# Optimization experiments

Measured on AMD Instinct MI355X. Metric: run time of the kernel, lower is better.

Reference implementation:

```python
import jax, jax.numpy as jnp
import numpy as np
from jax import lax

EPOCHS, P, IN_SIZE, OUT_SIZE = 3, 8, 32, 16
BS, C_EEG, T = 256, 22, 1000
DN = ('NCHW', 'OIHW', 'NCHW')


def _bn(h, g, b):
    # BatchNorm2d in training mode: biased batch stats over (N, H, W)
    mu = h.mean(axis=(0, 2, 3), keepdims=True)
    var = ((h - mu) ** 2).mean(axis=(0, 2, 3), keepdims=True)
    return (h - mu) * lax.rsqrt(var + 1e-5) * g.reshape(1, -1, 1, 1) + b.reshape(1, -1, 1, 1)


def _forward(x, conv1_w, conv1_b, bn1_g, bn1_b, conv2_w, conv2_b, bn2_g, bn2_b,
             wq, wk, wv, lin_w, lin_b):
    h = lax.conv_general_dilated(x, conv1_w, (1, 1), 'VALID', dimension_numbers=DN)
    h = jax.nn.elu(_bn(h + conv1_b.reshape(1, -1, 1, 1), bn1_g, bn1_b))          # (B,22,1,T)
    h = lax.conv_general_dilated(h, conv2_w, (1, 1), 'VALID', dimension_numbers=DN)
    h = jax.nn.elu(_bn(h + conv2_b.reshape(1, -1, 1, 1), bn2_g, bn2_b))          # (B,96,1,T-11)
    h = h[:, :, 0, :]                                                            # squeeze -> (B,96,T2)
    bs = h.shape[0]
    # E2R: split channel axis into EPOCHS equal patches, Projmap = X X^T
    X = h.reshape(bs, EPOCHS, IN_SIZE, -1)                                       # (B,m,32,T2)
    S = jnp.einsum('bmct,bmdt->bmcd', X, X)                                      # (B,m,32,32) SPD
    # Orthmap(p): top-p eigenvectors of S
    _, U = jnp.linalg.eigh(S)
    Up = U[..., ::-1][..., :P]                                                   # (B,m,32,8)
    # AttentionManifold: FRMap (W @ X) then QR composition -> orthonormal frames
    Q = jnp.linalg.qr(jnp.einsum('oi,bmip->bmop', wq, Up))[0]                    # (B,m,16,8)
    K = jnp.linalg.qr(jnp.einsum('oi,bmip->bmop', wk, Up))[0]
    V = jnp.linalg.qr(jnp.einsum('oi,bmip->bmop', wv, Up))[0]
    # projection-metric energy: E[b,i,j] = ||D D^T||_F with D = Q_j Q_j^T - K_i K_i^T
    QQt = jnp.einsum('bjdp,bjep->bjde', Q, Q)                                    # (B,m,16,16)
    KKt = jnp.einsum('bidp,biep->bide', K, K)
    D = QQt[:, None] - KKt[:, :, None]                                           # (B,i,j,16,16)
    E = jnp.sqrt(jnp.sum(jnp.matmul(D, jnp.swapaxes(D, -1, -2)) ** 2, axis=(-2, -1)))
    B = jax.nn.softmax(1.0 / (1.0 + jnp.log1p(E)), axis=1).transpose(0, 2, 1)    # (B,m,m)
    Vp = jnp.einsum('bmdp,bmep->bmde', V, V)                                     # Projmap(V)
    # faithful to the source triple loop: last j overwrites -> out[b,i] = B[b,i,-1] * Vp[b,-1]
    out = B[:, :, -1][:, :, None, None] * Vp[:, -1][:, None]                     # (B,m,16,16)
    return out.reshape(bs, -1) @ lin_w.T + lin_b                                 # (B,4)


def setup_inputs() -> dict:
    key = jax.random.key(0)
    ks = jax.random.split(key, 8)
    d2 = EPOCHS * IN_SIZE
    return {
        'x': jax.random.normal(ks[0], (BS, 1, C_EEG, T), jnp.float32),
        'conv1_w': jax.random.normal(ks[1], (C_EEG, 1, C_EEG, 1), jnp.float32) * 0.1,
        'conv1_b': jnp.zeros((C_EEG,), jnp.float32),
        'bn1_g': jnp.ones((C_EEG,), jnp.float32),
        'bn1_b': jnp.zeros((C_EEG,), jnp.float32),
        'conv2_w': jax.random.normal(ks[2], (d2, C_EEG, 1, 12), jnp.float32) * 0.05,
        'conv2_b': jnp.zeros((d2,), jnp.float32),
        'bn2_g': jnp.ones((d2,), jnp.float32),
        'bn2_b': jnp.zeros((d2,), jnp.float32),
        'wq': jax.random.normal(ks[3], (OUT_SIZE, IN_SIZE), jnp.float32) * 0.2,
        'wk': jax.random.normal(ks[4], (OUT_SIZE, IN_SIZE), jnp.float32) * 0.2,
        'wv': jax.random.normal(ks[5], (OUT_SIZE, IN_SIZE), jnp.float32) * 0.2,
        'lin_w': jax.random.normal(ks[6], (4, EPOCHS * OUT_SIZE * OUT_SIZE), jnp.float32) * 0.05,
        'lin_b': jnp.zeros((4,), jnp.float32),
    }


def reference(x, conv1_w, conv1_b, bn1_g, bn1_b, conv2_w, conv2_b, bn2_g, bn2_b,
              wq, wk, wv, lin_w, lin_b):
    return _forward(x, conv1_w, conv1_b, bn1_g, bn1_b, conv2_w, conv2_b, bn2_g, bn2_b,
                    wq, wk, wv, lin_w, lin_b)
```

## Files before the change

kernel.cpp:

```cpp
#include <hip/hip_runtime.h>
#include <math.h>

#define PDIM 8
#define BSZ 256
#define CEEG 22
#define TLEN 1000
#define KW 12
#define C2 96
#define TOUT 989
#define TSTR 992
#define NSWEEP 5
#define NT8 8
#define NPART (BSZ*NT8*2)

typedef __attribute__((ext_vector_type(8))) short short8;
typedef __attribute__((ext_vector_type(4))) float floatx4;

#define OFF_H1   ((size_t)0)
#define SZ_H1    ((size_t)BSZ*CEEG*TLEN)
#define OFF_H2   (OFF_H1 + SZ_H1)
#define SZ_H2    ((size_t)BSZ*C2*TSTR)
#define OFF_S    (OFF_H2 + SZ_H2)
#define SZ_S     ((size_t)BSZ*3*1024)
#define OFF_WH   (OFF_S)
#define OFF_WL   (OFF_S + (size_t)13824)
#define OFF_QQT  (OFF_S + SZ_S)
#define SZ_QQT   ((size_t)BSZ*3*256)
#define OFF_KKT  (OFF_QQT + SZ_QQT)
#define OFF_VP   (OFF_KKT + SZ_QQT)
#define SZ_VP    ((size_t)BSZ*256)
#define OFF_P1   (OFF_VP + SZ_VP)
#define SZ_P1    ((size_t)BSZ*44)
#define OFF_P2   (OFF_P1 + SZ_P1)
#define SZ_P2    ((size_t)NPART*192)
#define OFF_BN1  (OFF_P2 + SZ_P2)
#define OFF_BN2  (OFF_BN1 + (size_t)64)

__device__ __forceinline__ float elu_f(float z) { return z > 0.f ? z : expm1f(z); }

__device__ __forceinline__ unsigned short f2bf(float x) {
    unsigned u = __float_as_uint(x);
    u += 0x7fffu + ((u >> 16) & 1u);
    return (unsigned short)(u >> 16);
}
__device__ __forceinline__ float bf2f(unsigned short h) {
    return __uint_as_float(((unsigned)h) << 16);
}

__global__ __launch_bounds__(256) void k0_wsplit(const float* __restrict__ w2,
        unsigned short* __restrict__ Whi, unsigned short* __restrict__ Wlo) {
    int i = blockIdx.x*256 + threadIdx.x;
    if (i >= 96*288) return;
    int o = i / 288, kap = i - o*288;
    float v = (kap < 264) ? w2[o*264 + kap] : 0.f;
    unsigned short h = f2bf(v);
    float lo = v - bf2f(h);
    Whi[i] = h;
    Wlo[i] = f2bf(lo);
}

__global__ __launch_bounds__(256) void k1_conv1(const float* __restrict__ x,
        const float* __restrict__ w1, float* __restrict__ h1,
        float* __restrict__ part1) {
    __shared__ float sw[CEEG*CEEG];
    __shared__ float red[4][44];
    int b = blockIdx.x;
    int tid = threadIdx.x;
    for (int i = tid; i < CEEG*CEEG; i += 256) sw[i] = w1[i];
    __syncthreads();
    float sum[CEEG], sumsq[CEEG];
    #pragma unroll
    for (int o = 0; o < CEEG; ++o) { sum[o] = 0.f; sumsq[o] = 0.f; }
    const float* xb = x + (size_t)b*CEEG*TLEN;
    float* hb = h1 + (size_t)b*CEEG*TLEN;
    for (int it = 0; it < 4; ++it) {
        int t = it*256 + tid;
        if (t < TLEN) {
            float acc[CEEG];
            #pragma unroll
            for (int o = 0; o < CEEG; ++o) acc[o] = 0.f;
            #pragma unroll 2
            for (int c = 0; c < CEEG; ++c) {
                float xv = xb[c*TLEN + t];
                #pragma unroll
                for (int o = 0; o < CEEG; ++o) acc[o] = fmaf(xv, sw[o*CEEG + c], acc[o]);
            }
            #pragma unroll
            for (int o = 0; o < CEEG; ++o) {
                hb[o*TLEN + t] = acc[o];
                sum[o]  += acc[o];
                sumsq[o] += acc[o]*acc[o];
            }
        }
    }
    int lane = tid & 63, wv = tid >> 6;
    #pragma unroll
    for (int o = 0; o < CEEG; ++o) {
        float s = sum[o], s2 = sumsq[o];
        for (int off = 32; off > 0; off >>= 1) {
            s  += __shfl_down(s,  off, 64);
            s2 += __shfl_down(s2, off, 64);
        }
        if (lane == 0) { red[wv][o] = s; red[wv][CEEG + o] = s2; }
    }
    __syncthreads();
    if (tid < 44) {
        part1[(size_t)b*44 + tid] = red[0][tid] + red[1][tid] + red[2][tid] + red[3][tid];
    }
}

__global__ __launch_bounds__(64) void k2_bn1(const float* __restrict__ part1,
        const float* __restrict__ g, const float* __restrict__ bta, float* __restrict__ p1) {
    int c = blockIdx.x, t = threadIdx.x;
    float s = 0.f, s2 = 0.f;
    for (int blk = t; blk < BSZ; blk += 64) {
        s  += part1[(size_t)blk*44 + c];
        s2 += part1[(size_t)blk*44 + CEEG + c];
    }
    for (int off = 32; off > 0; off >>= 1) {
        s  += __shfl_down(s,  off, 64);
        s2 += __shfl_down(s2, off, 64);
    }
    if (t == 0) {
        double N = (double)BSZ * (double)TLEN;
        double mu = (double)s / N, var = (double)s2 / N - mu*mu;
        double scale = (double)g[c] / sqrt(var + 1e-5);
        p1[c] = (float)scale;
        p1[CEEG + c] = (float)((double)bta[c] - mu*scale);
    }
}

__global__ __launch_bounds__(256) void k3_conv2(const float* __restrict__ h1,
        const unsigned short* __restrict__ WhiG, const unsigned short* __restrict__ WloG,
        const float* __restrict__ p1, float* __restrict__ h2, float* __restrict__ part2) {
    __shared__ unsigned Epack[22*152];
    __shared__ unsigned short ctab[288];
    __shared__ short XhiL[128*40];
    __shared__ short XloL[128*40];
    int b = blockIdx.x;
    int tile = blockIdx.y;
    int t0 = tile * 128;
    int tid = threadIdx.x;
    int lane = tid & 63, w = tid >> 6;
    int r16 = lane & 15, q = lane >> 4;
    int mg = w & 1, ng = w >> 1;
    const float* hb = h1 + (size_t)b*CEEG*TLEN;

    for (int i = tid; i < 22*139; i += 256) {
        int c = i / 139, tt = i - c*139;
        int t = t0 + tt;
        unsigned pk = 0u;
        if (t < TLEN) {
            float v = elu_f(fmaf(hb[c*TLEN + t], p1[c], p1[CEEG + c]));
            unsigned uv = __float_as_uint(v);
            unsigned hi = uv & 0xFFFF0000u;
            float lo = v - __uint_as_float(hi);
            pk = hi | (__float_as_uint(lo) >> 16);
        }
        Epack[c*152 + tt] = pk;
    }
    for (int i = tid; i < 288; i += 256) {
        int c = i / 12, k = i - c*12;
        ctab[i] = (i < 264) ? (unsigned short)(c*152 + k) : (unsigned short)0xFFFF;
    }

    const unsigned short* ahP[3];
    const unsigned short* alP[3];
    #pragma unroll
    for (int m = 0; m < 3; ++m) {
        int row = mg*48 + m*16 + r16;
        ahP[m] = WhiG + row*288 + q*8;
        alP[m] = WloG + row*288 + q*8;
    }
    short8 ahC[3], alC[3];
    #pragma unroll
    for (int m = 0; m < 3; ++m) {
        ahC[m] = *(const short8*)&ahP[m][0];
        alC[m] = *(const short8*)&alP[m][0];
    }

    floatx4 acc[3][4];
    #pragma unroll
    for (int m = 0; m < 3; ++m)
        #pragma unroll
        for (int nf = 0; nf < 4; ++nf) acc[m][nf] = (floatx4){0.f, 0.f, 0.f, 0.f};

    __syncthreads();

    #pragma unroll
    for (int s = 0; s < 2; ++s) {
        int u = tid + s*256;
        int t = u >> 2, c4 = u & 3;
        const unsigned short* ct = &ctab[c4*8];
        unsigned dh[4], dl[4];
        #pragma unroll
        for (int jp = 0; jp < 4; ++jp) {
            unsigned short o0 = ct[2*jp], o1 = ct[2*jp+1];
            unsigned p0 = (o0 != 0xFFFFu) ? Epack[o0 + t] : 0u;
            unsigned p1v = (o1 != 0xFFFFu) ? Epack[o1 + t] : 0u;
            dh[jp] = (p0 >> 16) | (p1v & 0xFFFF0000u);
            dl[jp] = (p0 << 16 >> 16) | (p1v << 16);
        }
        *(uint4*)&XhiL[t*40 + c4*8] = make_uint4(dh[0], dh[1], dh[2], dh[3]);
        *(uint4*)&XloL[t*40 + c4*8] = make_uint4(dl[0], dl[1], dl[2], dl[3]);
    }
    __syncthreads();

    for (int kc = 0; kc < 9; ++kc) {
        short8 ahN[3], alN[3];
        if (kc + 1 < 9) {
            #pragma unroll
            for (int m = 0; m < 3; ++m) {
                ahN[m] = *(const short8*)&ahP[m][(kc+1)*32];
                alN[m] = *(const short8*)&alP[m][(kc+1)*32];
            }
        }
        #pragma unroll
        for (int nf = 0; nf < 4; ++nf) {
            int tn = (ng*4 + nf)*16 + r16;
            short8 bh = *(const short8*)&XhiL[tn*40 + q*8];
            short8 bl = *(const short8*)&XloL[tn*40 + q*8];
            #pragma unroll
            for (int m = 0; m < 3; ++m) {
                acc[m][nf] = __builtin_amdgcn_mfma_f32_16x16x32_bf16(ahC[m], bh, acc[m][nf], 0, 0, 0);
                acc[m][nf] = __builtin_amdgcn_mfma_f32_16x16x32_bf16(ahC[m], bl, acc[m][nf], 0, 0, 0);
                acc[m][nf] = __builtin_amdgcn_mfma_f32_16x16x32_bf16(alC[m], bh, acc[m][nf], 0, 0, 0);
            }
        }
        if (kc + 1 < 9) {
            __syncthreads();
            #pragma unroll
            for (int s = 0; s < 2; ++s) {
                int u = tid + s*256;
                int t = u >> 2, c4 = u & 3;
                const unsigned short* ct = &ctab[(kc+1)*32 + c4*8];
                unsigned dh[4], dl[4];
                #pragma unroll
                for (int jp = 0; jp < 4; ++jp) {
                    unsigned short o0 = ct[2*jp], o1 = ct[2*jp+1];
                    unsigned p0 = (o0 != 0xFFFFu) ? Epack[o0 + t] : 0u;
                    unsigned p1v = (o1 != 0xFFFFu) ? Epack[o1 + t] : 0u;
                    dh[jp] = (p0 >> 16) | (p1v & 0xFFFF0000u);
                    dl[jp] = (p0 << 16 >> 16) | (p1v << 16);
                }
                *(uint4*)&XhiL[t*40 + c4*8] = make_uint4(dh[0], dh[1], dh[2], dh[3]);
                *(uint4*)&XloL[t*40 + c4*8] = make_uint4(dl[0], dl[1], dl[2], dl[3]);
            }
            __syncthreads();
            #pragma unroll
            for (int m = 0; m < 3; ++m) { ahC[m] = ahN[m]; alC[m] = alN[m]; }
        }
    }

    float* h2b = h2 + (size_t)b*C2*TSTR;
    float* pb = part2 + (((size_t)b*NT8 + tile)*2 + ng)*192;
    #pragma unroll
    for (int m = 0; m < 3; ++m) {
        float s[4] = {0.f, 0.f, 0.f, 0.f}, s2[4] = {0.f, 0.f, 0.f, 0.f};
        #pragma unroll
        for (int nf = 0; nf < 4; ++nf) {
            int t = t0 + (ng*4 + nf)*16 + r16;
            bool ok = t < TOUT;
            #pragma unroll
            for (int reg = 0; reg < 4; ++reg) {
                float v = acc[m][nf][reg];
                if (ok) {
                    int o = mg*48 + m*16 + q*4 + reg;
                    h2b[(size_t)o*TSTR + t] = v;
                    s[reg] += v; s2[reg] += v*v;
                }
            }
        }
        #pragma unroll
        for (int reg = 0; reg < 4; ++reg) {
            float a = s[reg], b2 = s2[reg];
            #pragma unroll
            for (int d = 8; d > 0; d >>= 1) {
                a  += __shfl_down(a,  d, 16);
                b2 += __shfl_down(b2, d, 16);
            }
            if (r16 == 0) {
                int o = mg*48 + m*16 + q*4 + reg;
                pb[o] = a; pb[96 + o] = b2;
            }
        }
    }
}

__global__ __launch_bounds__(256) void k4_bn2(const float* __restrict__ part2,
        const float* __restrict__ g, const float* __restrict__ bta, float* __restrict__ p2) {
    __shared__ float rs[4], rs2[4];
    int q = blockIdx.x, t = threadIdx.x;
    float s = 0.f, s2 = 0.f;
    for (int blk = t; blk < NPART; blk += 256) {
        s  += part2[(size_t)blk*192 + q];
        s2 += part2[(size_t)blk*192 + 96 + q];
    }
    for (int off = 32; off > 0; off >>= 1) {
        s  += __shfl_down(s,  off, 64);
        s2 += __shfl_down(s2, off, 64);
    }
    int lane = t & 63, wv = t >> 6;
    if (lane == 0) { rs[wv] = s; rs2[wv] = s2; }
    __syncthreads();
    if (t == 0) {
        double S  = (double)rs[0]  + rs[1]  + rs[2]  + rs[3];
        double S2 = (double)rs2[0] + rs2[1] + rs2[2] + rs2[3];
        double N = (double)BSZ * (double)TOUT;
        double mu = S / N, var = S2 / N - mu*mu;
        double scale = (double)g[q] / sqrt(var + 1e-5);
        p2[q] = (float)scale;
        p2[C2 + q] = (float)((double)bta[q] - mu*scale);
    }
}

__global__ __launch_bounds__(256) void k5_gram(const float* __restrict__ h2,
        const float* __restrict__ p2, float* __restrict__ S) {
    __shared__ float smem[4*2176];
    int bm = blockIdx.x;
    int b = bm / 3, m = bm % 3;
    int tid = threadIdx.x;
    int w = tid >> 6, lane = tid & 63;
    float* sx = smem + w*2176;
    const float* hb = h2 + ((size_t)b*C2 + m*32)*TSTR;
    int srow = lane >> 1;
    int scol = (lane & 1) * 32;
    float sc = p2[m*32 + srow], sh = p2[C2 + m*32 + srow];
    int r0 = (lane >> 3) << 2, c0 = (lane & 7) << 2;
    float acc[4][4];
    #pragma unroll
    for (int i = 0; i < 4; ++i)
        #pragma unroll
        for (int j = 0; j < 4; ++j) acc[i][j] = 0.f;

    for (int t0 = w*64; t0 < TOUT; t0 += 256) {
        const float* src = &hb[(size_t)srow*TSTR + t0 + scol];
        float* drow = &sx[srow*68 + scol];
        if (t0 + 63 < TOUT) {
            #pragma unroll
            for (int j = 0; j < 8; ++j) {
                float4 xv = *(const float4*)&src[4*j];
                float4 v;
                v.x = elu_f(fmaf(xv.x, sc, sh));
                v.y = elu_f(fmaf(xv.y, sc, sh));
                v.z = elu_f(fmaf(xv.z, sc, sh));
                v.w = elu_f(fmaf(xv.w, sc, sh));
                *(float4*)&drow[4*j] = v;
            }
        } else {
            #pragma unroll
            for (int j = 0; j < 8; ++j) {
                float4 xv = *(const float4*)&src[4*j];
                int tb = t0 + scol + 4*j;
                float4 v;
                v.x = (tb + 0 < TOUT) ? elu_f(fmaf(xv.x, sc, sh)) : 0.f;
                v.y = (tb + 1 < TOUT) ? elu_f(fmaf(xv.y, sc, sh)) : 0.f;
                v.z = (tb + 2 < TOUT) ? elu_f(fmaf(xv.z, sc, sh)) : 0.f;
                v.w = (tb + 3 < TOUT) ? elu_f(fmaf(xv.w, sc, sh)) : 0.f;
                *(float4*)&drow[4*j] = v;
            }
        }
        #pragma unroll
        for (int tc = 0; tc < 16; ++tc) {
            float4 a0 = *(const float4*)&sx[(r0+0)*68 + tc*4];
            float4 a1 = *(const float4*)&sx[(r0+1)*68 + tc*4];
            float4 a2 = *(const float4*)&sx[(r0+2)*68 + tc*4];
            float4 a3 = *(const float4*)&sx[(r0+3)*68 + tc*4];
            float4 b0 = *(const float4*)&sx[(c0+0)*68 + tc*4];
            float4 b1 = *(const float4*)&sx[(c0+1)*68 + tc*4];
            float4 b2 = *(const float4*)&sx[(c0+2)*68 + tc*4];
            float4 b3 = *(const float4*)&sx[(c0+3)*68 + tc*4];
            #pragma unroll
            for (int i = 0; i < 4; ++i) {
                float4 ai = (i == 0) ? a0 : (i == 1) ? a1 : (i == 2) ? a2 : a3;
                acc[i][0] = fmaf(ai.x, b0.x, fmaf(ai.y, b0.y, fmaf(ai.z, b0.z, fmaf(ai.w, b0.w, acc[i][0]))));
                acc[i][1] = fmaf(ai.x, b1.x, fmaf(ai.y, b1.y, fmaf(ai.z, b1.z, fmaf(ai.w, b1.w, acc[i][1]))));
                acc[i][2] = fmaf(ai.x, b2.x, fmaf(ai.y, b2.y, fmaf(ai.z, b2.z, fmaf(ai.w, b2.w, acc[i][2]))));
                acc[i][3] = fmaf(ai.x, b3.x, fmaf(ai.y, b3.y, fmaf(ai.z, b3.z, fmaf(ai.w, b3.w, acc[i][3]))));
            }
        }
    }

    float* red = smem + w*2176;
    #pragma unroll
    for (int i = 0; i < 4; ++i)
        #pragma unroll
        for (int j = 0; j < 4; ++j)
            red[lane*17 + i*4 + j] = acc[i][j];
    __syncthreads();
    int e0 = tid * 4;
    int r = e0 >> 5, c = e0 & 31;
    int tl = (r >> 2)*8 + (c >> 2);
    int sb = (r & 3)*4;
    float o0 = 0.f, o1 = 0.f, o2 = 0.f, o3 = 0.f;
    #pragma unroll
    for (int ww = 0; ww < 4; ++ww) {
        const float* rp = smem + ww*2176 + tl*17 + sb;
        o0 += rp[0]; o1 += rp[1]; o2 += rp[2]; o3 += rp[3];
    }
    float* Sb2 = S + (size_t)bm*1024;
    *(float4*)&Sb2[e0] = make_float4(o0, o1, o2, o3);
}

__device__ __forceinline__ void pair_of(int r, int k, int& p, int& q) {
    if (k == 0) { p = r; q = 31; }
    else {
        int a = (r + k) % 31;
        int b2 = (r - k + 31) % 31;
        p = min(a, b2); q = max(a, b2);
    }
}

__global__ __launch_bounds__(256) void k6_eig(const float* __restrict__ S,
        const float* __restrict__ wq, const float* __restrict__ wk, const float* __restrict__ wv,
        float* __restrict__ QQt, float* __restrict__ KKt, float* __restrict__ Vp) {
    __shared__ float A[32][35];
    __shared__ float Vt[32][34];
    __shared__ float2 cs2[16];
    __shared__ float sW[3][512];
    __shared__ unsigned int ptab[31*16];
    __shared__ float Up[32][9];
    __shared__ float Aw[16][9];
    __shared__ float G[8][9];
    __shared__ float Lm[8][9];
    __shared__ float Mm[16][9];
    __shared__ float lam[32];
    int bm = blockIdx.x, b = bm / 3, m = bm % 3;
    int tid = threadIdx.x;
    const float* Sb = S + (size_t)bm*1024;
    for (int i = tid; i < 1024; i += 256) {
        int r_ = i >> 5, c_ = i & 31;
        A[r_][c_] = Sb[i];
        Vt[r_][c_] = (r_ == c_) ? 1.f : 0.f;
    }
    for (int i = tid; i < 512; i += 256) {
        sW[0][i] = wq[i]; sW[1][i] = wk[i]; sW[2][i] = wv[i];
    }
    for (int i = tid; i < 31*16; i += 256) {
        int r_ = i >> 4, k_ = i & 15;
        int p, q; pair_of(r_, k_, p, q);
        ptab[i] = (unsigned)p | ((unsigned)q << 16);
    }
    __syncthreads();

    int kk_ = tid >> 4, ll_ = tid & 15;
    int i0 = kk_ * 2;
    for (int sweep = 0; sweep < NSWEEP; ++sweep) {
        for (int r = 0; r < 31; ++r) {
            if (tid < 16) {
                unsigned pq = ptab[(r << 4) + tid];
                int p = pq & 0xffff, q = pq >> 16;
                float app = A[p][p], aqq = A[q][q], apq = A[p][q];
                float c = 1.f, s = 0.f;
                if (apq != 0.f) {
                    float tau = (aqq - app) / (2.f * apq);
                    float tt = (tau >= 0.f ? 1.f : -1.f) / (fabsf(tau) + sqrtf(1.f + tau*tau));
                    c = 1.f / sqrtf(1.f + tt*tt);
                    s = tt * c;
                    if (!(c == c) || !(s == s)) { c = 1.f; s = 0.f; }
                }
                cs2[tid] = make_float2(c, s);
            }
            __syncthreads();
            {
                unsigned pqk = ptab[(r << 4) + kk_];
                unsigned pql = ptab[(r << 4) + ll_];
                int p = pqk & 0xffff, q = pqk >> 16;
                int rr = pql & 0xffff, ss = pql >> 16;
                float2 ck2 = cs2[kk_], cl2 = cs2[ll_];
                float ck = ck2.x, sk = ck2.y, cl = cl2.x, sl = cl2.y;
                float apr = A[p][rr], aps = A[p][ss], aqr = A[q][rr], aqs = A[q][ss];
                float tpr = ck*apr - sk*aqr;
                float tqr = sk*apr + ck*aqr;
                float tps = ck*aps - sk*aqs;
                float tqs = sk*aps + ck*aqs;
                A[p][rr] = cl*tpr - sl*tps;
                A[p][ss] = sl*tpr + cl*tps;
                A[q][rr] = cl*tqr - sl*tqs;
                A[q][ss] = sl*tqr + cl*tqs;
                float2 vr = *(const float2*)&Vt[rr][i0];
                float2 vs = *(const float2*)&Vt[ss][i0];
                float2 nvr, nvs;
                nvr.x = cl*vr.x - sl*vs.x;
                nvr.y = cl*vr.y - sl*vs.y;
                nvs.x = sl*vr.x + cl*vs.x;
                nvs.y = sl*vr.y + cl*vs.y;
                *(float2*)&Vt[rr][i0] = nvr;
                *(float2*)&Vt[ss][i0] = nvs;
            }
            __syncthreads();
        }
    }

    if (tid < 32) lam[tid] = A[tid][tid];
    __syncthreads();
    if (tid < 32) {
        float lj = lam[tid];
        int rank = 0;
        #pragma unroll
        for (int i = 0; i < 32; ++i) {
            float li = lam[i];
            rank += (li > lj) || (li == lj && i < tid);
        }
        if (rank < PDIM) {
            #pragma unroll
            for (int i = 0; i < 32; ++i) Up[i][rank] = Vt[tid][i];
        }
    }
    __syncthreads();

    for (int widx = 0; widx < 3; ++widx) {
        if (widx == 2 && m != 2) break;
        const float* W = sW[widx];
        if (tid < 128) {
            int o = tid >> 3, pp = tid & 7;
            float s = 0.f;
            #pragma unroll
            for (int i = 0; i < 32; ++i) s = fmaf(W[o*32 + i], Up[i][pp], s);
            Aw[o][pp] = s;
        }
        __syncthreads();
        if (tid < 64) {
            int xx = tid >> 3, yy = tid & 7;
            float s = 0.f;
            #pragma unroll
            for (int o = 0; o < 16; ++o) s = fmaf(Aw[o][xx], Aw[o][yy], s);
            G[xx][yy] = s;
        }
        __syncthreads();
        if (tid == 0) {
            float Lr[8][8];
            #pragma unroll
            for (int jj = 0; jj < 8; ++jj) {
                float d = G[jj][jj];
                #pragma unroll
                for (int kk = 0; kk < 8; ++kk) if (kk < jj) d -= Lr[jj][kk]*Lr[jj][kk];
                d = sqrtf(fmaxf(d, 1e-30f));
                float inv = 1.f / d;
                Lr[jj][jj] = d;
                Lm[jj][jj] = inv;
                #pragma unroll
                for (int ii = 0; ii < 8; ++ii) if (ii > jj) {
                    float v = G[ii][jj];
                    #pragma unroll
                    for (int kk = 0; kk < 8; ++kk) if (kk < jj) v -= Lr[ii][kk]*Lr[jj][kk];
                    v *= inv;
                    Lr[ii][jj] = v;
                    Lm[ii][jj] = v;
                }
            }
        }
        __syncthreads();
        if (tid < 16) {
            int o = tid;
            float a[8], mv[8];
            #pragma unroll
            for (int pp = 0; pp < 8; ++pp) a[pp] = Aw[o][pp];
            #pragma unroll
            for (int jj = 0; jj < 8; ++jj) {
                float v = a[jj];
                #pragma unroll
                for (int kk = 0; kk < 8; ++kk) if (kk < jj) v -= Lm[jj][kk]*mv[kk];
                mv[jj] = v * Lm[jj][jj];
            }
            #pragma unroll
            for (int pp = 0; pp < 8; ++pp) Mm[o][pp] = mv[pp];
        }
        __syncthreads();
        {
            int d = tid >> 4, e = tid & 15;
            float s = 0.f;
            #pragma unroll
            for (int pp = 0; pp < 8; ++pp) s = fmaf(Mm[d][pp], Mm[e][pp], s);
            float* dst = (widx == 0) ? (QQt + (size_t)bm*256)
                       : (widx == 1) ? (KKt + (size_t)bm*256)
                       : (Vp + (size_t)b*256);
            dst[d*16 + e] = s;
        }
        __syncthreads();
    }
}

__global__ __launch_bounds__(64) void k7_out(const float* __restrict__ QQt,
        const float* __restrict__ KKt, const float* __restrict__ Vp,
        const float* __restrict__ lw, const float* __restrict__ lb,
        float* __restrict__ out) {
    __shared__ float sQ[3][256], sK[3][256], sVp[256], ssc[9], wj[3];
    int b = blockIdx.x, tid = threadIdx.x;
    for (int i = tid; i < 768; i += 64) {
        sQ[i >> 8][i & 255] = QQt[(size_t)b*768 + i];
        sK[i >> 8][i & 255] = KKt[(size_t)b*768 + i];
    }
    for (int i = tid; i < 256; i += 64) sVp[i] = Vp[(size_t)b*256 + i];
    __syncthreads();
    for (int pair = 0; pair < 9; ++pair) {
        int i = pair / 3, j = pair % 3;
        const float* Qj = sQ[j];
        const float* Ki = sK[i];
        float accp = 0.f;
        #pragma unroll
        for (int it = 0; it < 4; ++it) {
            int e = tid + 64*it;
            int d = e >> 4, ee = e & 15;
            float y = 0.f;
            #pragma unroll
            for (int f = 0; f < 16; ++f) {
                float dv = Qj[d*16 + f] - Ki[d*16 + f];
                float ev = Qj[ee*16 + f] - Ki[ee*16 + f];
                y = fmaf(dv, ev, y);
            }
            accp += y*y;
        }
        for (int off = 32; off > 0; off >>= 1) accp += __shfl_down(accp, off, 64);
        if (tid == 0) {
            float E = sqrtf(accp);
            ssc[pair] = 1.f / (1.f + log1pf(E));
        }
        __syncthreads();
    }
    if (tid < 3) {
        int j = tid;
        float e0 = expf(ssc[0*3 + j]), e1 = expf(ssc[1*3 + j]), e2 = expf(ssc[2*3 + j]);
        wj[j] = e2 / (e0 + e1 + e2);
    }
    __syncthreads();
    int o = tid >> 4, g = tid & 15;
    float part = 0.f;
    #pragma unroll
    for (int t = 0; t < 16; ++t) {
        int de = g*16 + t;
        float vv = sVp[de];
        float l0 = lw[o*768 + de];
        float l1 = lw[o*768 + 256 + de];
        float l2 = lw[o*768 + 512 + de];
        part = fmaf(vv, fmaf(wj[0], l0, fmaf(wj[1], l1, wj[2]*l2)), part);
    }
    for (int off = 8; off > 0; off >>= 1) part += __shfl_down(part, off, 16);
    if (g == 0) out[b*4 + o] = part + lb[o];
}

extern "C" void kernel_launch(void* const* d_in, const int* in_sizes, int n_in,
                              void* d_out, int out_size, void* d_ws, size_t ws_size,
                              hipStream_t stream) {
    const float* x  = (const float*)d_in[0];
    const float* w1 = (const float*)d_in[1];
    const float* g1 = (const float*)d_in[3];
    const float* b1 = (const float*)d_in[4];
    const float* w2 = (const float*)d_in[5];
    const float* g2 = (const float*)d_in[7];
    const float* b2 = (const float*)d_in[8];
    const float* wq = (const float*)d_in[9];
    const float* wk = (const float*)d_in[10];
    const float* wv = (const float*)d_in[11];
    const float* lw = (const float*)d_in[12];
    const float* lb = (const float*)d_in[13];

    float* ws   = (float*)d_ws;
    float* h1   = ws + OFF_H1;
    float* h2   = ws + OFF_H2;
    float* Sm   = ws + OFF_S;
    unsigned short* WhiG = (unsigned short*)(ws + OFF_WH);
    unsigned short* WloG = (unsigned short*)(ws + OFF_WL);
    float* qqt  = ws + OFF_QQT;
    float* kkt  = ws + OFF_KKT;
    float* vpm  = ws + OFF_VP;
    float* p1a  = ws + OFF_P1;
    float* p2a  = ws + OFF_P2;
    float* bn1p = ws + OFF_BN1;
    float* bn2p = ws + OFF_BN2;

    k0_wsplit<<<(96*288 + 255)/256, 256, 0, stream>>>(w2, WhiG, WloG);
    k1_conv1<<<BSZ, 256, 0, stream>>>(x, w1, h1, p1a);
    k2_bn1<<<CEEG, 64, 0, stream>>>(p1a, g1, b1, bn1p);
    dim3 g3(BSZ, NT8);
    k3_conv2<<<g3, 256, 0, stream>>>(h1, WhiG, WloG, bn1p, h2, p2a);
    k4_bn2<<<C2, 256, 0, stream>>>(p2a, g2, b2, bn2p);
    k5_gram<<<BSZ*3, 256, 0, stream>>>(h2, bn2p, Sm);
    k6_eig<<<BSZ*3, 256, 0, stream>>>(Sm, wq, wk, wv, qqt, kkt, vpm);
    k7_out<<<BSZ, 64, 0, stream>>>(qqt, kkt, vpm, lw, lb, (float*)d_out);
}
```

Measured before the change: 386.4 us.

## Shrink Jacobi eigen kernel to a single 64-thread wavefront per matrix

Runs the per-matrix Jacobi eigensolver with 64 threads (one wavefront) instead of 256. Each thread now applies four column rotations, and the downstream FRMap, Gram and outer-product steps are remapped to fit 64 threads. The intent is to make the two block barriers per rotation round cheap, since a single-wave block needs no cross-wave synchronisation, and to fit more blocks per CU. In exchange each thread does serial work per round and there is less parallelism inside a block.

```diff
diff --git a/kernel.cpp b/kernel.cpp
--- a/kernel.cpp
+++ b/kernel.cpp
@@ -411,7 +411,7 @@
     }
 }
 
-__global__ __launch_bounds__(256) void k6_eig(const float* __restrict__ S,
+__global__ __launch_bounds__(64) void k6_eig(const float* __restrict__ S,
         const float* __restrict__ wq, const float* __restrict__ wk, const float* __restrict__ wv,
         float* __restrict__ QQt, float* __restrict__ KKt, float* __restrict__ Vp) {
     __shared__ float A[32][35];
@@ -428,29 +428,30 @@
     int bm = blockIdx.x, b = bm / 3, m = bm % 3;
     int tid = threadIdx.x;
     const float* Sb = S + (size_t)bm*1024;
-    for (int i = tid; i < 1024; i += 256) {
+    for (int i = tid; i < 1024; i += 64) {
         int r_ = i >> 5, c_ = i & 31;
         A[r_][c_] = Sb[i];
         Vt[r_][c_] = (r_ == c_) ? 1.f : 0.f;
     }
-    for (int i = tid; i < 512; i += 256) {
+    for (int i = tid; i < 512; i += 64) {
         sW[0][i] = wq[i]; sW[1][i] = wk[i]; sW[2][i] = wv[i];
     }
-    for (int i = tid; i < 31*16; i += 256) {
+    for (int i = tid; i < 31*16; i += 64) {
         int r_ = i >> 4, k_ = i & 15;
         int p, q; pair_of(r_, k_, p, q);
         ptab[i] = (unsigned)p | ((unsigned)q << 16);
     }
     __syncthreads();
 
-    int kk_ = tid >> 4, ll_ = tid & 15;
-    int i0 = kk_ * 2;
+    int kk = tid >> 2, j4 = tid & 3;
+    int i0 = kk * 2;
     for (int sweep = 0; sweep < NSWEEP; ++sweep) {
         for (int r = 0; r < 31; ++r) {
-            if (tid < 16) {
-                unsigned pq = ptab[(r << 4) + tid];
-                int p = pq & 0xffff, q = pq >> 16;
-                float app = A[p][p], aqq = A[q][q], apq = A[p][q];
+            const unsigned* pt = &ptab[r << 4];
+            {
+                unsigned pq = pt[tid & 15];
+                int p_ = pq & 0xffff, q_ = pq >> 16;
+                float app = A[p_][p_], aqq = A[q_][q_], apq = A[p_][q_];
                 float c = 1.f, s = 0.f;
                 if (apq != 0.f) {
                     float tau = (aqq - app) / (2.f * apq);
@@ -459,34 +460,40 @@
                     s = tt * c;
                     if (!(c == c) || !(s == s)) { c = 1.f; s = 0.f; }
                 }
-                cs2[tid] = make_float2(c, s);
+                if (tid < 16) cs2[tid] = make_float2(c, s);
             }
             __syncthreads();
             {
-                unsigned pqk = ptab[(r << 4) + kk_];
-                unsigned pql = ptab[(r << 4) + ll_];
+                unsigned pqk = pt[kk];
                 int p = pqk & 0xffff, q = pqk >> 16;
-                int rr = pql & 0xffff, ss = pql >> 16;
-                float2 ck2 = cs2[kk_], cl2 = cs2[ll_];
-                float ck = ck2.x, sk = ck2.y, cl = cl2.x, sl = cl2.y;
-                float apr = A[p][rr], aps = A[p][ss], aqr = A[q][rr], aqs = A[q][ss];
-                float tpr = ck*apr - sk*aqr;
-                float tqr = sk*apr + ck*aqr;
-                float tps = ck*aps - sk*aqs;
-                float tqs = sk*aps + ck*aqs;
-                A[p][rr] = cl*tpr - sl*tps;
-                A[p][ss] = sl*tpr + cl*tps;
-                A[q][rr] = cl*tqr - sl*tqs;
-                A[q][ss] = sl*tqr + cl*tqs;
-                float2 vr = *(const float2*)&Vt[rr][i0];
-                float2 vs = *(const float2*)&Vt[ss][i0];
-                float2 nvr, nvs;
-                nvr.x = cl*vr.x - sl*vs.x;
-                nvr.y = cl*vr.y - sl*vs.y;
-                nvs.x = sl*vr.x + cl*vs.x;
-                nvs.y = sl*vr.y + cl*vs.y;
-                *(float2*)&Vt[rr][i0] = nvr;
-                *(float2*)&Vt[ss][i0] = nvs;
+                float2 csk = cs2[kk];
+                float ck = csk.x, sk = csk.y;
+                #pragma unroll
+                for (int s5 = 0; s5 < 4; ++s5) {
+                    int ll = j4 * 4 + s5;
+                    unsigned pql = pt[ll];
+                    int rr = pql & 0xffff, ss = pql >> 16;
+                    float2 csl = cs2[ll];
+                    float cl = csl.x, sl = csl.y;
+                    float apr = A[p][rr], aps = A[p][ss], aqr = A[q][rr], aqs = A[q][ss];
+                    float tpr = ck*apr - sk*aqr;
+                    float tqr = sk*apr + ck*aqr;
+                    float tps = ck*aps - sk*aqs;
+                    float tqs = sk*aps + ck*aqs;
+                    A[p][rr] = cl*tpr - sl*tps;
+                    A[p][ss] = sl*tpr + cl*tps;
+                    A[q][rr] = cl*tqr - sl*tqs;
+                    A[q][ss] = sl*tqr + cl*tqs;
+                    float2 vr = *(const float2*)&Vt[rr][i0];
+                    float2 vs = *(const float2*)&Vt[ss][i0];
+                    float2 nvr, nvs;
+                    nvr.x = cl*vr.x - sl*vs.x;
+                    nvr.y = cl*vr.y - sl*vs.y;
+                    nvs.x = sl*vr.x + cl*vs.x;
+                    nvs.y = sl*vr.y + cl*vs.y;
+                    *(float2*)&Vt[rr][i0] = nvr;
+                    *(float2*)&Vt[ss][i0] = nvs;
+                }
             }
             __syncthreads();
         }
@@ -512,15 +519,20 @@
     for (int widx = 0; widx < 3; ++widx) {
         if (widx == 2 && m != 2) break;
         const float* W = sW[widx];
-        if (tid < 128) {
+        {
             int o = tid >> 3, pp = tid & 7;
-            float s = 0.f;
-            #pragma unroll
-            for (int i = 0; i < 32; ++i) s = fmaf(W[o*32 + i], Up[i][pp], s);
-            Aw[o][pp] = s;
+            float s0 = 0.f, s1 = 0.f;
+            #pragma unroll
+            for (int i = 0; i < 32; ++i) {
+                float u = Up[i][pp];
+                s0 = fmaf(W[o*32 + i], u, s0);
+                s1 = fmaf(W[(o+8)*32 + i], u, s1);
+            }
+            Aw[o][pp] = s0;
+            Aw[o+8][pp] = s1;
         }
         __syncthreads();
-        if (tid < 64) {
+        {
             int xx = tid >> 3, yy = tid & 7;
             float s = 0.f;
             #pragma unroll
@@ -534,7 +546,7 @@
             for (int jj = 0; jj < 8; ++jj) {
                 float d = G[jj][jj];
                 #pragma unroll
-                for (int kk = 0; kk < 8; ++kk) if (kk < jj) d -= Lr[jj][kk]*Lr[jj][kk];
+                for (int kk2 = 0; kk2 < 8; ++kk2) if (kk2 < jj) d -= Lr[jj][kk2]*Lr[jj][kk2];
                 d = sqrtf(fmaxf(d, 1e-30f));
                 float inv = 1.f / d;
                 Lr[jj][jj] = d;
@@ -543,7 +555,7 @@
                 for (int ii = 0; ii < 8; ++ii) if (ii > jj) {
                     float v = G[ii][jj];
                     #pragma unroll
-                    for (int kk = 0; kk < 8; ++kk) if (kk < jj) v -= Lr[ii][kk]*Lr[jj][kk];
+                    for (int kk2 = 0; kk2 < 8; ++kk2) if (kk2 < jj) v -= Lr[ii][kk2]*Lr[jj][kk2];
                     v *= inv;
                     Lr[ii][jj] = v;
                     Lm[ii][jj] = v;
@@ -560,7 +572,7 @@
             for (int jj = 0; jj < 8; ++jj) {
                 float v = a[jj];
                 #pragma unroll
-                for (int kk = 0; kk < 8; ++kk) if (kk < jj) v -= Lm[jj][kk]*mv[kk];
+                for (int kk2 = 0; kk2 < 8; ++kk2) if (kk2 < jj) v -= Lm[jj][kk2]*mv[kk2];
                 mv[jj] = v * Lm[jj][jj];
             }
             #pragma unroll
@@ -568,14 +580,18 @@
         }
         __syncthreads();
         {
-            int d = tid >> 4, e = tid & 15;
-            float s = 0.f;
-            #pragma unroll
-            for (int pp = 0; pp < 8; ++pp) s = fmaf(Mm[d][pp], Mm[e][pp], s);
             float* dst = (widx == 0) ? (QQt + (size_t)bm*256)
                        : (widx == 1) ? (KKt + (size_t)bm*256)
                        : (Vp + (size_t)b*256);
-            dst[d*16 + e] = s;
+            #pragma unroll
+            for (int t4 = 0; t4 < 4; ++t4) {
+                int e = tid + 64*t4;
+                int d = e >> 4, ee = e & 15;
+                float s = 0.f;
+                #pragma unroll
+                for (int pp = 0; pp < 8; ++pp) s = fmaf(Mm[d][pp], Mm[ee][pp], s);
+                dst[e] = s;
+            }
         }
         __syncthreads();
     }
@@ -676,6 +692,6 @@
     k3_conv2<<<g3, 256, 0, stream>>>(h1, WhiG, WloG, bn1p, h2, p2a);
     k4_bn2<<<C2, 256, 0, stream>>>(p2a, g2, b2, bn2p);
     k5_gram<<<BSZ*3, 256, 0, stream>>>(h2, bn2p, Sm);
-    k6_eig<<<BSZ*3, 256, 0, stream>>>(Sm, wq, wk, wv, qqt, kkt, vpm);
+    k6_eig<<<BSZ*3, 64, 0, stream>>>(Sm, wq, wk, wv, qqt, kkt, vpm);
     k7_out<<<BSZ, 64, 0, stream>>>(qqt, kkt, vpm, lw, lb, (float*)d_out);
 }
```

New measurement: 431.3 us. +11.6%, slower.
